# Kernel optimization log

Measured on AMD Instinct MI355X. Metric: run time of the kernel, lower is better.

## Reference

```python
import jax, jax.numpy as jnp
import numpy as np

D_MODEL = 1024
N_HEADS = 16
N_GROUPS = 4
CONTEXT_LEN = 512
D_H = D_MODEL // N_HEADS          # 64
GROUP_SIZE = N_HEADS // N_GROUPS  # 4
B, S = 4, 2048


def setup_inputs() -> dict:
    key = jax.random.key(0)
    ks = jax.random.split(key, 9)
    s = 0.02
    return {
        "x": jax.random.normal(ks[0], (B, S, D_MODEL), dtype=jnp.float32),
        "Wq": jax.random.normal(ks[1], (D_MODEL, D_MODEL), dtype=jnp.float32) * s,
        "bq": jax.random.normal(ks[2], (D_MODEL,), dtype=jnp.float32) * s,
        "Wk": jax.random.normal(ks[3], (D_MODEL, N_GROUPS * D_H), dtype=jnp.float32) * s,
        "bk": jax.random.normal(ks[4], (N_GROUPS * D_H,), dtype=jnp.float32) * s,
        "Wv": jax.random.normal(ks[5], (D_MODEL, N_GROUPS * D_H), dtype=jnp.float32) * s,
        "bv": jax.random.normal(ks[6], (N_GROUPS * D_H,), dtype=jnp.float32) * s,
        "Wo": jax.random.normal(ks[7], (D_MODEL, D_MODEL), dtype=jnp.float32) * s,
        "bo": jax.random.normal(ks[8], (D_MODEL,), dtype=jnp.float32) * s,
    }


def reference(x, Wq, bq, Wk, bk, Wv, bv, Wo, bo):
    b, s = x.shape[0], x.shape[1]
    # Projections. q: [b, n_groups, group_size, s, d_h]; k/v: [b, n_groups, s, d_h]
    q = (x @ Wq + bq).reshape(b, s, N_GROUPS, GROUP_SIZE, D_H)
    q = jnp.transpose(q, (0, 2, 3, 1, 4))
    k = jnp.transpose((x @ Wk + bk).reshape(b, s, N_GROUPS, D_H), (0, 2, 1, 3))
    v = jnp.transpose((x @ Wv + bv).reshape(b, s, N_GROUPS, D_H), (0, 2, 1, 3))
    # Grouped scores (einsum broadcast == repeat_interleave of k over group_size)
    scores = jnp.einsum("bghqd,bgkd->bghqk", q, k) / jnp.sqrt(jnp.float32(D_H))
    # Sliding-window causal mask (cached_len == s when use_cache=False)
    i = jnp.arange(s)
    j = jnp.arange(s)
    upper = (i - CONTEXT_LEN)[:, None] >= j[None, :]   # too-old keys
    lower = i[:, None] < j[None, :]                    # future keys
    mask = upper | lower                               # [s, s]
    scores = jnp.where(mask, jnp.float32(-1e9), scores)
    att = jax.nn.softmax(scores, axis=-1)
    out = jnp.einsum("bghqk,bgkd->bghqd", att, v)      # [b, g, h, s, d_h]
    out = jnp.transpose(out, (0, 3, 1, 2, 4)).reshape(b, s, D_MODEL)
    return out @ Wo + bo
```

## Files before the change

kernel.cpp:

```cpp
#include <hip/hip_runtime.h>
#include <cstdint>
#include <cstddef>

typedef __attribute__((ext_vector_type(8))) short short8;
typedef __attribute__((ext_vector_type(4))) short short4v;
typedef __attribute__((ext_vector_type(4))) float f32x4;
typedef __attribute__((ext_vector_type(4))) unsigned short ushort4v;
typedef __attribute__((ext_vector_type(4))) unsigned int uint4v;
typedef unsigned short ushort_t;

union Frag8 { short4v h[2]; short8 v; };
union PFrag { unsigned int w[4]; short8 v; };

__device__ __forceinline__ ushort_t f2bf(float f) {
  unsigned int u = __builtin_bit_cast(unsigned int, f);
  u += 0x7FFFu + ((u >> 16) & 1u);
  return (ushort_t)(u >> 16);
}

__device__ __forceinline__ void gload16(const void* g, void* l) {
  __builtin_amdgcn_global_load_lds(
      (const __attribute__((address_space(1))) unsigned int*)g,
      (__attribute__((address_space(3))) unsigned int*)l, 16, 0, 0);
}

__device__ __forceinline__ void cvt8(const float4& a, const float4& b, uint4v& o) {
  asm("v_cvt_pk_bf16_f32 %0, %1, %2" : "=v"(o.x) : "v"(a.x), "v"(a.y));
  asm("v_cvt_pk_bf16_f32 %0, %1, %2" : "=v"(o.y) : "v"(a.z), "v"(a.w));
  asm("v_cvt_pk_bf16_f32 %0, %1, %2" : "=v"(o.z) : "v"(b.x), "v"(b.y));
  asm("v_cvt_pk_bf16_f32 %0, %1, %2" : "=v"(o.w) : "v"(b.z), "v"(b.w));
}

__global__ __launch_bounds__(256) void transpose_w_kernel(
    const float* __restrict__ Wq, const float* __restrict__ Wk,
    const float* __restrict__ Wv, const float* __restrict__ Wo,
    ushort_t* __restrict__ Wt) {
  __shared__ float tile[32][33];
  const int tn = blockIdx.x, tk = blockIdx.y;
  const int n0 = tn * 32;
  const float* W; int ldn, nloc;
  if      (n0 < 1024) { W = Wq; ldn = 1024; nloc = n0; }
  else if (n0 < 1280) { W = Wk; ldn = 256;  nloc = n0 - 1024; }
  else if (n0 < 1536) { W = Wv; ldn = 256;  nloc = n0 - 1280; }
  else                { W = Wo; ldn = 1024; nloc = n0 - 1536; }
  const int t = threadIdx.x;
  const int sr = t >> 3, sc = (t & 7) * 4;
  const float4 v = *reinterpret_cast<const float4*>(W + (size_t)(tk * 32 + sr) * ldn + nloc + sc);
  tile[sr][sc] = v.x; tile[sr][sc + 1] = v.y; tile[sr][sc + 2] = v.z; tile[sr][sc + 3] = v.w;
  __syncthreads();
  const int wr = t >> 3, wc = (t & 7) * 4;
  ushort4v o = { f2bf(tile[wc][wr]), f2bf(tile[wc + 1][wr]),
                 f2bf(tile[wc + 2][wr]), f2bf(tile[wc + 3][wr]) };
  *reinterpret_cast<ushort4v*>(Wt + (size_t)(n0 + wr) * 1024 + tk * 32 + wc) = o;
}

__global__ void prep_bias_kernel(const float* __restrict__ bq, const float* __restrict__ bk,
                                 const float* __restrict__ bv, float* __restrict__ bqkv) {
  int t = blockIdx.x * 256 + threadIdx.x;
  if (t < 1536) bqkv[t] = (t < 1024) ? bq[t] : (t < 1280) ? bk[t - 1024] : bv[t - 1280];
}

#define GEMM_IDS \
  const int tid = threadIdx.x;                        \
  const int w = tid >> 6, lane = tid & 63;            \
  const int wm = w >> 1, wn = w & 1;                  \
  const int g = lane >> 4, r16 = lane & 15;

#define GEMM_KLOOP(APTR, BPTR)                                                          \
  const f32x4 vzero = {0.f, 0.f, 0.f, 0.f};                                             \
  f32x4 acc[4][4];                                                                      \
  _Pragma("unroll") for (int i = 0; i < 4; ++i)                                         \
    _Pragma("unroll") for (int j = 0; j < 4; ++j) acc[i][j] = vzero;                    \
  auto stage = [&](int s, int k0) {                                                     \
    char* base = LdsB + s * 16384;                                                      \
    _Pragma("unroll") for (int i = 0; i < 2; ++i) {                                     \
      const int u = tid + i * 256;                                                      \
      const int row = u >> 2;                                                           \
      const int pu = (u & 3) ^ ((u >> 3) & 3);                                          \
      gload16((const char*)(APTR) + (size_t)(bm * 128 + row) * 2048 + k0 * 2 + pu * 16, \
              base + u * 16);                                                           \
    }                                                                                   \
    _Pragma("unroll") for (int i = 0; i < 2; ++i) {                                     \
      const int u = tid + i * 256;                                                      \
      const int row = u >> 2;                                                           \
      const int pu = (u & 3) ^ ((u >> 3) & 3);                                          \
      gload16((const char*)(BPTR) + (size_t)(bn * 128 + row) * 2048 + k0 * 2 + pu * 16, \
              base + 8192 + u * 16);                                                    \
    }                                                                                   \
  };                                                                                    \
  stage(0, 0);                                                                          \
  stage(1, 32);                                                                         \
  const int fsw = (g ^ ((r16 >> 1) & 3)) << 4;                                          \
  for (int t = 0; t < 32; ++t) {                                                        \
    if (t < 31) { asm volatile("s_waitcnt vmcnt(4) lgkmcnt(0)" ::: "memory"); }         \
    else        { asm volatile("s_waitcnt vmcnt(0) lgkmcnt(0)" ::: "memory"); }         \
    __builtin_amdgcn_s_barrier();                                                       \
    if (t + 2 < 32) stage((t + 2) % 3, (t + 2) * 32);                                   \
    const char* Ab = LdsB + (t % 3) * 16384;                                            \
    const char* Bb = Ab + 8192;                                                         \
    short8 af[4], bf[4];                                                                \
    _Pragma("unroll") for (int mi = 0; mi < 4; ++mi)                                    \
      af[mi] = *(const short8*)(Ab + (wm * 64 + mi * 16 + r16) * 64 + fsw);             \
    _Pragma("unroll") for (int ni = 0; ni < 4; ++ni)                                    \
      bf[ni] = *(const short8*)(Bb + (wn * 64 + ni * 16 + r16) * 64 + fsw);             \
    __builtin_amdgcn_s_setprio(1);                                                      \
    _Pragma("unroll") for (int mi = 0; mi < 4; ++mi)                                    \
      _Pragma("unroll") for (int ni = 0; ni < 4; ++ni)                                  \
        acc[mi][ni] = __builtin_amdgcn_mfma_f32_16x16x32_bf16(af[mi], bf[ni], acc[mi][ni], 0, 0, 0); \
    __builtin_amdgcn_s_setprio(0);                                                      \
  }

__global__ __launch_bounds__(256, 3) void gemm_qkv_kernel(
    const float* __restrict__ X, const ushort_t* __restrict__ Bt,
    const float* __restrict__ bias,
    ushort_t* __restrict__ Qb, ushort_t* __restrict__ Kb, ushort_t* __restrict__ Vt)
{
  __shared__ __align__(16) char LdsB[49152];
  const int xcd = blockIdx.x & 7, ii = blockIdx.x >> 3;
  const int bm = xcd * 8 + ii / 12, bn = ii % 12;
  GEMM_IDS

  const f32x4 vzero = {0.f, 0.f, 0.f, 0.f};
  f32x4 acc[4][4];
#pragma unroll
  for (int i = 0; i < 4; ++i)
#pragma unroll
    for (int j = 0; j < 4; ++j) acc[i][j] = vzero;

  const int arow = tid >> 1;
  const int alu0 = (tid & 1) * 2;
  const int asw  = (arow >> 1) & 3;
  const float* aptr = X + (size_t)(bm * 128 + arow) * 1024 + alu0 * 8;
  char* const awr = LdsB  + arow * 64;

  auto issueA = [&](int k0, float4* r) {
    const float* p = aptr + k0;
#pragma unroll
    for (int i = 0; i < 4; ++i) r[i] = *reinterpret_cast<const float4*>(p + i * 4);
  };
  auto issueB = [&](int s, int k0) {
    char* base = LdsB + s * 16384 + 8192;
#pragma unroll
    for (int i = 0; i < 2; ++i) {
      const int u = tid + i * 256;
      const int row = u >> 2;
      const int pu = (u & 3) ^ ((u >> 3) & 3);
      gload16((const char*)Bt + (size_t)(bn * 128 + row) * 2048 + k0 * 2 + pu * 16,
              base + u * 16);
    }
  };
  auto writeA = [&](int s, const float4* r) {
    char* base = awr + s * 16384;
    uint4v p0, p1;
    cvt8(r[0], r[1], p0);
    cvt8(r[2], r[3], p1);
    *reinterpret_cast<uint4v*>(base + ((alu0 ^ asw) << 4)) = p0;
    *reinterpret_cast<uint4v*>(base + (((alu0 + 1) ^ asw) << 4)) = p1;
  };

  float4 rA0[4], rA1[4];
  issueB(0, 0);  issueA(0, rA0);
  issueB(1, 32); issueA(32, rA1);
  asm volatile("s_waitcnt vmcnt(6)" ::: "memory");
  writeA(0, rA0);

  const int fsw = (g ^ ((r16 >> 1) & 3)) << 4;
  auto iter = [&](int t, float4* rIssue, float4* rWrite) {
    asm volatile("s_waitcnt lgkmcnt(0)" ::: "memory");
    __builtin_amdgcn_s_barrier();
    if (t + 2 < 32) { issueB((t + 2) % 3, (t + 2) * 32); issueA((t + 2) * 32, rIssue); }
    const char* Ab = LdsB + (t % 3) * 16384;
    const char* Bb = Ab + 8192;
    short8 af[4], bf[4];
#pragma unroll
    for (int mi = 0; mi < 4; ++mi)
      af[mi] = *(const short8*)(Ab + (wm * 64 + mi * 16 + r16) * 64 + fsw);
#pragma unroll
    for (int ni = 0; ni < 4; ++ni)
      bf[ni] = *(const short8*)(Bb + (wn * 64 + ni * 16 + r16) * 64 + fsw);
    __builtin_amdgcn_s_setprio(1);
#pragma unroll
    for (int mi = 0; mi < 4; ++mi)
#pragma unroll
      for (int ni = 0; ni < 4; ++ni)
        acc[mi][ni] = __builtin_amdgcn_mfma_f32_16x16x32_bf16(af[mi], bf[ni], acc[mi][ni], 0, 0, 0);
    __builtin_amdgcn_s_setprio(0);
    __builtin_amdgcn_sched_barrier(0);
    if (t + 1 < 32) {
      if (t + 2 < 32) { asm volatile("s_waitcnt vmcnt(6)" ::: "memory"); }
      else            { asm volatile("s_waitcnt vmcnt(0)" ::: "memory"); }
      writeA((t + 1) % 3, rWrite);
    }
  };
  for (int tt = 0; tt < 16; ++tt) {
    iter(2 * tt,     rA0, rA1);
    iter(2 * tt + 1, rA1, rA0);
  }

  float bcol[4];
#pragma unroll
  for (int ni = 0; ni < 4; ++ni) bcol[ni] = bias[bn * 128 + wn * 64 + ni * 16 + r16];
  if (bn < 8) {
#pragma unroll
    for (int mi = 0; mi < 4; ++mi)
#pragma unroll
      for (int ni = 0; ni < 4; ++ni) {
        const int col = bn * 128 + wn * 64 + ni * 16 + r16;
#pragma unroll
        for (int rr = 0; rr < 4; ++rr) {
          const int row = bm * 128 + wm * 64 + mi * 16 + g * 4 + rr;
          Qb[(size_t)row * 1024 + col] = f2bf((acc[mi][ni][rr] + bcol[ni]) * 0.180336881f);
        }
      }
  } else if (bn < 10) {
#pragma unroll
    for (int mi = 0; mi < 4; ++mi)
#pragma unroll
      for (int ni = 0; ni < 4; ++ni) {
        const int c = bn * 128 + wn * 64 + ni * 16 + r16 - 1024;
        const int gi = c >> 6, dd = c & 63;
#pragma unroll
        for (int rr = 0; rr < 4; ++rr) {
          const int row = bm * 128 + wm * 64 + mi * 16 + g * 4 + rr;
          const int bb = row >> 11, s = row & 2047;
          Kb[((size_t)(bb * 4 + gi) * 2048 + s) * 64 + dd] = f2bf(acc[mi][ni][rr] + bcol[ni]);
        }
      }
  } else {
#pragma unroll
    for (int mi = 0; mi < 4; ++mi) {
      const int row0 = bm * 128 + wm * 64 + mi * 16 + g * 4;
      const int bb = row0 >> 11;
      const int s = row0 & 2047;
      const int pos = (s & ~31) + g * 8 + (mi & 1) * 4;
#pragma unroll
      for (int ni = 0; ni < 4; ++ni) {
        const int c = bn * 128 + wn * 64 + ni * 16 + r16 - 1280;
        const int gi = c >> 6, dd = c & 63;
        ushort4v pk;
#pragma unroll
        for (int rr = 0; rr < 4; ++rr) pk[rr] = f2bf(acc[mi][ni][rr] + bcol[ni]);
        *reinterpret_cast<ushort4v*>(Vt + ((size_t)(bb * 4 + gi) * 64 + dd) * 2048 + pos) = pk;
      }
    }
  }
}

__global__ __launch_bounds__(256, 3) void gemm_out_kernel(
    const ushort_t* __restrict__ A, const ushort_t* __restrict__ Bt,
    const float* __restrict__ bias, float* __restrict__ Cout)
{
  __shared__ __align__(16) char LdsB[49152];
  const int xcd = blockIdx.x & 7, ii = blockIdx.x >> 3;
  const int bm = xcd * 8 + (ii >> 3), bn = ii & 7;
  GEMM_IDS
  GEMM_KLOOP(A, Bt)

  float bcol[4];
#pragma unroll
  for (int ni = 0; ni < 4; ++ni) bcol[ni] = bias[bn * 128 + wn * 64 + ni * 16 + r16];
#pragma unroll
  for (int mi = 0; mi < 4; ++mi)
#pragma unroll
    for (int ni = 0; ni < 4; ++ni) {
      const int col = bn * 128 + wn * 64 + ni * 16 + r16;
#pragma unroll
      for (int rr = 0; rr < 4; ++rr) {
        const int row = bm * 128 + wm * 64 + mi * 16 + g * 4 + rr;
        Cout[(size_t)row * 1024 + col] = acc[mi][ni][rr] + bcol[ni];
      }
    }
}

__global__ __launch_bounds__(512, 2) void attn_kernel(
    const ushort_t* __restrict__ Qb, const ushort_t* __restrict__ Kb,
    const ushort_t* __restrict__ Vt, ushort_t* __restrict__ attout)
{
  __shared__ __align__(16) char KsB[24576];
  __shared__ __align__(16) char VsB[24576];
  const int fid = blockIdx.x;
  const int lo = fid & 7, hi = fid >> 3;
  const int qt = 31 - (hi & 31);
  const int gbsel = lo | ((hi >> 5) << 3);
  const int gg = gbsel & 3, b = gbsel >> 2;

  const int tid = threadIdx.x;
  const int w = tid >> 6, lane = tid & 63;
  const int hw = w & 3, qh = w >> 2;
  const int h = gg * 4 + hw;
  const int g = lane >> 4, r16 = lane & 15;
  const int q0w = qt * 64 + qh * 32;

  short8 qf[2][2];
#pragma unroll
  for (int qs = 0; qs < 2; ++qs) {
    const char* qptr = (const char*)Qb + ((size_t)(b * 2048 + q0w + qs * 16 + r16) * 1024 + h * 64) * 2;
#pragma unroll
    for (int dc = 0; dc < 2; ++dc)
      qf[qs][dc] = *(const short8*)(qptr + dc * 64 + g * 16);
  }

  const f32x4 vzero = {0.f, 0.f, 0.f, 0.f};
  f32x4 accO[2][4];
#pragma unroll
  for (int qs = 0; qs < 2; ++qs)
#pragma unroll
    for (int nt = 0; nt < 4; ++nt) accO[qs][nt] = vzero;
  float lsum[2] = {0.f, 0.f};

  const char* KbB = (const char*)Kb + (size_t)(b * 4 + gg) * 2048 * 128;
  const char* VtB = (const char*)Vt + (size_t)(b * 4 + gg) * 64 * 4096;

  const int kb0 = (qt >= 8) ? (qt * 64 - 512) : 0;
  const int NT = (qt * 64 + 64 - kb0) >> 6;

  const int srr = tid >> 3, spk = tid & 7;
  auto stage = [&](int buf, int kb) {
    gload16(KbB + (size_t)(kb + srr) * 128 + ((spk ^ (srr & 7)) << 4),
            KsB + buf * 8192 + tid * 16);
    gload16(VtB + (size_t)srr * 4096 + (size_t)kb * 2 + ((spk ^ (srr & 7)) << 4),
            VsB + buf * 8192 + tid * 16);
  };

  stage(0, kb0);
  if (NT > 1) stage(1, kb0 + 64);
  for (int t = 0; t < NT; ++t) {
    if (t < NT - 1) { asm volatile("s_waitcnt vmcnt(2) lgkmcnt(0)" ::: "memory"); }
    else            { asm volatile("s_waitcnt vmcnt(0) lgkmcnt(0)" ::: "memory"); }
    __builtin_amdgcn_s_barrier();
    if (t + 2 < NT) stage((t + 2) % 3, kb0 + (t + 2) * 64);
    const int kb = kb0 + t * 64;
    const char* Ks = KsB + (t % 3) * 8192;
    const char* Vs = VsB + (t % 3) * 8192;

    f32x4 st[2][4];
#pragma unroll
    for (int ki = 0; ki < 4; ++ki) {
      const int key = ki * 16 + r16;
      const int swz = key & 7;
      const short8 kf0 = *(const short8*)(Ks + key * 128 + ((g ^ swz) << 4));
      const short8 kf1 = *(const short8*)(Ks + key * 128 + (((4 + g) ^ swz) << 4));
#pragma unroll
      for (int qs = 0; qs < 2; ++qs) {
        st[qs][ki] = __builtin_amdgcn_mfma_f32_16x16x32_bf16(kf0, qf[qs][0], vzero, 0, 0, 0);
        st[qs][ki] = __builtin_amdgcn_mfma_f32_16x16x32_bf16(kf1, qf[qs][1], st[qs][ki], 0, 0, 0);
      }
    }

    const bool full = (kb >= q0w - 480) && (kb <= q0w - 63);
    PFrag pf[2][2];
    if (full) {
#pragma unroll
      for (int qs = 0; qs < 2; ++qs) {
#pragma unroll
        for (int ki = 0; ki < 4; ++ki)
#pragma unroll
          for (int r = 0; r < 4; ++r)
            st[qs][ki][r] = __builtin_amdgcn_exp2f(st[qs][ki][r]);
      }
    } else {
#pragma unroll
      for (int qs = 0; qs < 2; ++qs) {
        const int q = q0w + qs * 16 + r16;
#pragma unroll
        for (int ki = 0; ki < 4; ++ki)
#pragma unroll
          for (int r = 0; r < 4; ++r) {
            const int key = kb + ki * 16 + g * 4 + r;
            const bool valid = (key <= q) && (key + 512 > q);
            st[qs][ki][r] = __builtin_amdgcn_exp2f(valid ? st[qs][ki][r] : -INFINITY);
          }
      }
    }
#pragma unroll
    for (int qs = 0; qs < 2; ++qs) {
      float tk[4];
#pragma unroll
      for (int ki = 0; ki < 4; ++ki)
        tk[ki] = (st[qs][ki][0] + st[qs][ki][1]) + (st[qs][ki][2] + st[qs][ki][3]);
      lsum[qs] += (tk[0] + tk[1]) + (tk[2] + tk[3]);
#pragma unroll
      for (int c = 0; c < 2; ++c)
#pragma unroll
        for (int pr = 0; pr < 2; ++pr) {
          asm("v_cvt_pk_bf16_f32 %0, %1, %2"
              : "=v"(pf[qs][c].w[pr * 2])
              : "v"(st[qs][2 * c + pr][0]), "v"(st[qs][2 * c + pr][1]));
          asm("v_cvt_pk_bf16_f32 %0, %1, %2"
              : "=v"(pf[qs][c].w[pr * 2 + 1])
              : "v"(st[qs][2 * c + pr][2]), "v"(st[qs][2 * c + pr][3]));
        }
    }

#pragma unroll
    for (int c = 0; c < 2; ++c)
#pragma unroll
      for (int nt = 0; nt < 4; ++nt) {
        const int d = nt * 16 + r16;
        const short8 vf = *(const short8*)(Vs + d * 128 + (((c * 4 + g) ^ (d & 7)) << 4));
#pragma unroll
        for (int qs = 0; qs < 2; ++qs)
          accO[qs][nt] = __builtin_amdgcn_mfma_f32_16x16x32_bf16(pf[qs][c].v, vf, accO[qs][nt], 0, 0, 0);
      }
  }

#pragma unroll
  for (int qs = 0; qs < 2; ++qs) {
    float ts = lsum[qs];
    ts += __shfl_xor(ts, 16);
    ts += __shfl_xor(ts, 32);
    const float linv = 1.f / ts;
    float lq[4];
#pragma unroll
    for (int rr = 0; rr < 4; ++rr) lq[rr] = __shfl(linv, g * 4 + rr);
#pragma unroll
    for (int nt = 0; nt < 4; ++nt) {
      const int ocol = h * 64 + nt * 16 + r16;
#pragma unroll
      for (int rr = 0; rr < 4; ++rr) {
        const int orow = b * 2048 + q0w + qs * 16 + g * 4 + rr;
        attout[(size_t)orow * 1024 + ocol] = f2bf(accO[qs][nt][rr] * lq[rr]);
      }
    }
  }
}

extern "C" void kernel_launch(void* const* d_in, const int* in_sizes, int n_in,
                              void* d_out, int out_size, void* d_ws, size_t ws_size,
                              hipStream_t stream) {
  (void)in_sizes; (void)n_in; (void)out_size; (void)ws_size;
  const float* x  = (const float*)d_in[0];
  const float* Wq = (const float*)d_in[1];
  const float* bq = (const float*)d_in[2];
  const float* Wk = (const float*)d_in[3];
  const float* bk = (const float*)d_in[4];
  const float* Wv = (const float*)d_in[5];
  const float* bv = (const float*)d_in[6];
  const float* Wo = (const float*)d_in[7];
  const float* bo = (const float*)d_in[8];

  char* ws = (char*)d_ws;
  ushort_t* Qb   = (ushort_t*)(ws + 0);
  ushort_t* Kb   = (ushort_t*)(ws + 16777216);
  ushort_t* Vt   = (ushort_t*)(ws + 20971520);
  ushort_t* wt   = (ushort_t*)(ws + 25165824);
  float*    bqkv = (float*)   (ws + 30408704);
  ushort_t* att  = (ushort_t*)(ws + 47194112);

  transpose_w_kernel<<<dim3(80, 32), 256, 0, stream>>>(Wq, Wk, Wv, Wo, wt);
  prep_bias_kernel<<<6, 256, 0, stream>>>(bq, bk, bv, bqkv);
  gemm_qkv_kernel<<<768, 256, 0, stream>>>(x, wt, bqkv, Qb, Kb, Vt);
  attn_kernel<<<512, 512, 0, stream>>>(Qb, Kb, Vt, att);
  gemm_out_kernel<<<512, 256, 0, stream>>>(att, wt + (size_t)1536 * 1024, bo, (float*)d_out);
}
```

Measured before the change: 106.7 us.

## Stage fp32 X tile directly into LDS via async loads, convert at fragment read

The QKV GEMM stops loading X fp32 into registers, converting to bf16 and writing LDS. It now issues async global-to-LDS loads of the fp32 tile with an XOR swizzle and converts to bf16 when reading MFMA fragments. The LDS footprint grows to 72KB, so occupancy drops from 3 to 2 blocks per CU. The bias-prep kernel is also folded into the weight transpose kernel to remove one launch. The trade is fewer VGPRs and a simpler pipeline against doubled LDS traffic for A and lower occupancy.

```diff
diff --git a/kernel.cpp b/kernel.cpp
--- a/kernel.cpp
+++ b/kernel.cpp
@@ -11,6 +11,7 @@
 
 union Frag8 { short4v h[2]; short8 v; };
 union PFrag { unsigned int w[4]; short8 v; };
+union AFrag { uint4v u; short8 v; };
 
 __device__ __forceinline__ ushort_t f2bf(float f) {
   unsigned int u = __builtin_bit_cast(unsigned int, f);
@@ -24,19 +25,18 @@
       (__attribute__((address_space(3))) unsigned int*)l, 16, 0, 0);
 }
 
-__device__ __forceinline__ void cvt8(const float4& a, const float4& b, uint4v& o) {
-  asm("v_cvt_pk_bf16_f32 %0, %1, %2" : "=v"(o.x) : "v"(a.x), "v"(a.y));
-  asm("v_cvt_pk_bf16_f32 %0, %1, %2" : "=v"(o.y) : "v"(a.z), "v"(a.w));
-  asm("v_cvt_pk_bf16_f32 %0, %1, %2" : "=v"(o.z) : "v"(b.x), "v"(b.y));
-  asm("v_cvt_pk_bf16_f32 %0, %1, %2" : "=v"(o.w) : "v"(b.z), "v"(b.w));
-}
-
 __global__ __launch_bounds__(256) void transpose_w_kernel(
     const float* __restrict__ Wq, const float* __restrict__ Wk,
     const float* __restrict__ Wv, const float* __restrict__ Wo,
-    ushort_t* __restrict__ Wt) {
+    const float* __restrict__ bq, const float* __restrict__ bk,
+    const float* __restrict__ bv, ushort_t* __restrict__ Wt,
+    float* __restrict__ bqkv) {
   __shared__ float tile[32][33];
   const int tn = blockIdx.x, tk = blockIdx.y;
+  if (tk == 0) {
+    const int t = tn * 256 + threadIdx.x;
+    if (t < 1536) bqkv[t] = (t < 1024) ? bq[t] : (t < 1280) ? bk[t - 1024] : bv[t - 1280];
+  }
   const int n0 = tn * 32;
   const float* W; int ldn, nloc;
   if      (n0 < 1024) { W = Wq; ldn = 1024; nloc = n0; }
@@ -52,12 +52,6 @@
   ushort4v o = { f2bf(tile[wc][wr]), f2bf(tile[wc + 1][wr]),
                  f2bf(tile[wc + 2][wr]), f2bf(tile[wc + 3][wr]) };
   *reinterpret_cast<ushort4v*>(Wt + (size_t)(n0 + wr) * 1024 + tk * 32 + wc) = o;
-}
-
-__global__ void prep_bias_kernel(const float* __restrict__ bq, const float* __restrict__ bk,
-                                 const float* __restrict__ bv, float* __restrict__ bqkv) {
-  int t = blockIdx.x * 256 + threadIdx.x;
-  if (t < 1536) bqkv[t] = (t < 1024) ? bq[t] : (t < 1280) ? bk[t - 1024] : bv[t - 1280];
 }
 
 #define GEMM_IDS \
@@ -110,12 +104,12 @@
     __builtin_amdgcn_s_setprio(0);                                                      \
   }
 
-__global__ __launch_bounds__(256, 3) void gemm_qkv_kernel(
+__global__ __launch_bounds__(256, 2) void gemm_qkv_kernel(
     const float* __restrict__ X, const ushort_t* __restrict__ Bt,
     const float* __restrict__ bias,
     ushort_t* __restrict__ Qb, ushort_t* __restrict__ Kb, ushort_t* __restrict__ Vt)
 {
-  __shared__ __align__(16) char LdsB[49152];
+  __shared__ __align__(16) char LdsB[73728];
   const int xcd = blockIdx.x & 7, ii = blockIdx.x >> 3;
   const int bm = xcd * 8 + ii / 12, bn = ii % 12;
   GEMM_IDS
@@ -127,54 +121,50 @@
 #pragma unroll
     for (int j = 0; j < 4; ++j) acc[i][j] = vzero;
 
-  const int arow = tid >> 1;
-  const int alu0 = (tid & 1) * 2;
-  const int asw  = (arow >> 1) & 3;
-  const float* aptr = X + (size_t)(bm * 128 + arow) * 1024 + alu0 * 8;
-  char* const awr = LdsB  + arow * 64;
-
-  auto issueA = [&](int k0, float4* r) {
-    const float* p = aptr + k0;
-#pragma unroll
-    for (int i = 0; i < 4; ++i) r[i] = *reinterpret_cast<const float4*>(p + i * 4);
-  };
-  auto issueB = [&](int s, int k0) {
-    char* base = LdsB + s * 16384 + 8192;
+  auto stage = [&](int s, int k0) {
+    char* base = LdsB + s * 24576;
+#pragma unroll
+    for (int i = 0; i < 4; ++i) {
+      const int u = tid + i * 256;
+      const int row = u >> 3, phys = u & 7;
+      gload16((const char*)X + (size_t)(bm * 128 + row) * 4096 + k0 * 4
+                  + ((phys ^ (row & 7)) << 4),
+              base + u * 16);
+    }
 #pragma unroll
     for (int i = 0; i < 2; ++i) {
       const int u = tid + i * 256;
       const int row = u >> 2;
       const int pu = (u & 3) ^ ((u >> 3) & 3);
       gload16((const char*)Bt + (size_t)(bn * 128 + row) * 2048 + k0 * 2 + pu * 16,
-              base + u * 16);
+              base + 16384 + u * 16);
     }
   };
-  auto writeA = [&](int s, const float4* r) {
-    char* base = awr + s * 16384;
-    uint4v p0, p1;
-    cvt8(r[0], r[1], p0);
-    cvt8(r[2], r[3], p1);
-    *reinterpret_cast<uint4v*>(base + ((alu0 ^ asw) << 4)) = p0;
-    *reinterpret_cast<uint4v*>(base + (((alu0 + 1) ^ asw) << 4)) = p1;
-  };
-
-  float4 rA0[4], rA1[4];
-  issueB(0, 0);  issueA(0, rA0);
-  issueB(1, 32); issueA(32, rA1);
-  asm volatile("s_waitcnt vmcnt(6)" ::: "memory");
-  writeA(0, rA0);
-
+
+  stage(0, 0);
+  stage(1, 32);
   const int fsw = (g ^ ((r16 >> 1) & 3)) << 4;
-  auto iter = [&](int t, float4* rIssue, float4* rWrite) {
-    asm volatile("s_waitcnt lgkmcnt(0)" ::: "memory");
+  const int s7 = r16 & 7;
+  for (int t = 0; t < 32; ++t) {
+    if (t < 31) { asm volatile("s_waitcnt vmcnt(6) lgkmcnt(0)" ::: "memory"); }
+    else        { asm volatile("s_waitcnt vmcnt(0) lgkmcnt(0)" ::: "memory"); }
     __builtin_amdgcn_s_barrier();
-    if (t + 2 < 32) { issueB((t + 2) % 3, (t + 2) * 32); issueA((t + 2) * 32, rIssue); }
-    const char* Ab = LdsB + (t % 3) * 16384;
-    const char* Bb = Ab + 8192;
+    if (t + 2 < 32) stage((t + 2) % 3, (t + 2) * 32);
+    const char* Ab = LdsB + (t % 3) * 24576;
+    const char* Bb = Ab + 16384;
     short8 af[4], bf[4];
 #pragma unroll
-    for (int mi = 0; mi < 4; ++mi)
-      af[mi] = *(const short8*)(Ab + (wm * 64 + mi * 16 + r16) * 64 + fsw);
+    for (int mi = 0; mi < 4; ++mi) {
+      const int row = wm * 64 + mi * 16 + r16;
+      const f32x4 v0 = *(const f32x4*)(Ab + row * 128 + (((2 * g) ^ s7) << 4));
+      const f32x4 v1 = *(const f32x4*)(Ab + row * 128 + (((2 * g + 1) ^ s7) << 4));
+      AFrag fa;
+      asm("v_cvt_pk_bf16_f32 %0, %1, %2" : "=v"(fa.u.x) : "v"(v0[0]), "v"(v0[1]));
+      asm("v_cvt_pk_bf16_f32 %0, %1, %2" : "=v"(fa.u.y) : "v"(v0[2]), "v"(v0[3]));
+      asm("v_cvt_pk_bf16_f32 %0, %1, %2" : "=v"(fa.u.z) : "v"(v1[0]), "v"(v1[1]));
+      asm("v_cvt_pk_bf16_f32 %0, %1, %2" : "=v"(fa.u.w) : "v"(v1[2]), "v"(v1[3]));
+      af[mi] = fa.v;
+    }
 #pragma unroll
     for (int ni = 0; ni < 4; ++ni)
       bf[ni] = *(const short8*)(Bb + (wn * 64 + ni * 16 + r16) * 64 + fsw);
@@ -185,16 +175,6 @@
       for (int ni = 0; ni < 4; ++ni)
         acc[mi][ni] = __builtin_amdgcn_mfma_f32_16x16x32_bf16(af[mi], bf[ni], acc[mi][ni], 0, 0, 0);
     __builtin_amdgcn_s_setprio(0);
-    __builtin_amdgcn_sched_barrier(0);
-    if (t + 1 < 32) {
-      if (t + 2 < 32) { asm volatile("s_waitcnt vmcnt(6)" ::: "memory"); }
-      else            { asm volatile("s_waitcnt vmcnt(0)" ::: "memory"); }
-      writeA((t + 1) % 3, rWrite);
-    }
-  };
-  for (int tt = 0; tt < 16; ++tt) {
-    iter(2 * tt,     rA0, rA1);
-    iter(2 * tt + 1, rA1, rA0);
   }
 
   float bcol[4];
@@ -447,8 +427,7 @@
   float*    bqkv = (float*)   (ws + 30408704);
   ushort_t* att  = (ushort_t*)(ws + 47194112);
 
-  transpose_w_kernel<<<dim3(80, 32), 256, 0, stream>>>(Wq, Wk, Wv, Wo, wt);
-  prep_bias_kernel<<<6, 256, 0, stream>>>(bq, bk, bv, bqkv);
+  transpose_w_kernel<<<dim3(80, 32), 256, 0, stream>>>(Wq, Wk, Wv, Wo, bq, bk, bv, wt, bqkv);
   gemm_qkv_kernel<<<768, 256, 0, stream>>>(x, wt, bqkv, Qb, Kb, Vt);
   attn_kernel<<<512, 512, 0, stream>>>(Qb, Kb, Vt, att);
   gemm_out_kernel<<<512, 256, 0, stream>>>(att, wt + (size_t)1536 * 1024, bo, (float*)d_out);
```

Measured after the change: 103.9 us. 1.03x faster.
